# Performance work log

Measured on AMD Instinct MI355X. Metric: run time of the kernel, lower is better.

## Reference

```python
import jax, jax.numpy as jnp
import numpy as np

D_MODEL = 768
N_HEAD = 12


def setup_inputs() -> dict:
    key = jax.random.key(0)
    ks = jax.random.split(key, 5)
    B, S, D = 2, 4096, D_MODEL
    scale = 0.02
    return {
        "x": jax.random.normal(ks[0], (B, S, D), dtype=jnp.float32),
        "W_in": jax.random.normal(ks[1], (D, 3 * D), dtype=jnp.float32) * scale,
        "b_in": jax.random.normal(ks[2], (3 * D,), dtype=jnp.float32) * scale,
        "W_out": jax.random.normal(ks[3], (D, D), dtype=jnp.float32) * scale,
        "b_out": jax.random.normal(ks[4], (D,), dtype=jnp.float32) * scale,
    }


def reference(x, W_in, b_in, W_out, b_out):
    B, S, D = x.shape
    H = N_HEAD
    d_head = D // H
    qkv = x @ W_in + b_in                      # [B,S,3D]
    q, k, v = jnp.split(qkv, 3, axis=-1)
    # [B,H,S,d]
    q = q.reshape(B, S, H, d_head).transpose(0, 2, 1, 3)
    k = k.reshape(B, S, H, d_head).transpose(0, 2, 1, 3)
    v = v.reshape(B, S, H, d_head).transpose(0, 2, 1, 3)
    att = jnp.einsum("bhqd,bhkd->bhqk", q, k) * (1.0 / jnp.sqrt(jnp.float32(d_head)))
    causal = jnp.tril(jnp.ones((S, S), dtype=bool))
    att = jnp.where(causal[None, None], att, jnp.float32(-jnp.inf))
    att = jax.nn.softmax(att, axis=-1)
    y = jnp.einsum("bhqk,bhkd->bhqd", att, v)  # [B,H,S,d]
    y = y.transpose(0, 2, 1, 3).reshape(B, S, D)
    return y @ W_out + b_out
```

## Files before the change

### kernel.cpp

```cpp
#include <hip/hip_runtime.h>
#include <hip/hip_bf16.h>


#define D_MODEL 768
#define SEQ 4096
#define NB 2
#define NHEAD 12
#define LDQK 1536

typedef __attribute__((ext_vector_type(8))) short short8;
typedef __attribute__((ext_vector_type(4))) float floatx4;
typedef __attribute__((ext_vector_type(16))) float floatx16;

#define SM_C 0.18033688011112042f

#if __has_builtin(__builtin_amdgcn_exp2f)
#define EXP2(x) __builtin_amdgcn_exp2f(x)
#else
#define EXP2(x) __expf((x) * 0.6931471805599453f)
#endif

__device__ inline short fb(float f) {
    union { __hip_bfloat16 h; short s; } cv;
    cv.h = __float2bfloat16(f);
    return cv.s;
}
__device__ inline unsigned pk2(float a, float b) {
    float2 f; f.x = a; f.y = b;
    union { __hip_bfloat162 h; unsigned u; } cv;
    cv.h = __float22bfloat162_rn(f);
    return cv.u;
}
__device__ inline void gload16(const void* g, void* l) {
    __builtin_amdgcn_global_load_lds(
        (const __attribute__((address_space(1))) unsigned int*)g,
        (__attribute__((address_space(3))) unsigned int*)l, 16, 0, 0);
}

__global__ __launch_bounds__(256) void convert_bf16(const float* __restrict__ src,
                                                    short* __restrict__ dst, size_t n) {
    size_t i = ((size_t)blockIdx.x * 256 + threadIdx.x) * 8;
    if (i >= n) return;
    float4 f0 = *(const float4*)(src + i);
    float4 f1 = *(const float4*)(src + i + 4);
    uint4 u = {pk2(f0.x, f0.y), pk2(f0.z, f0.w), pk2(f1.x, f1.y), pk2(f1.z, f1.w)};
    *(uint4*)(dst + i) = u;
}

__global__ __launch_bounds__(256) void transpose_bf16(const float* __restrict__ W,
                                                      short* __restrict__ Wt,
                                                      int K, int N) {
    __shared__ short t[32][33];
    const int n0 = blockIdx.x * 32, k0 = blockIdx.y * 32;
    const int tx = threadIdx.x, ty = threadIdx.y;
#pragma unroll
    for (int j = 0; j < 4; ++j)
        t[ty + j * 8][tx] = fb(W[(size_t)(k0 + ty + j * 8) * N + n0 + tx]);
    __syncthreads();
#pragma unroll
    for (int j = 0; j < 4; ++j)
        Wt[(size_t)(n0 + ty + j * 8) * K + k0 + tx] = t[tx][ty + j * 8];
}

__global__ __launch_bounds__(256) void gemm_qkv128(const short* __restrict__ A,
                                                   const short* __restrict__ Bt,
                                                   const float* __restrict__ bias,
                                                   short* __restrict__ qkw,
                                                   short* __restrict__ vtw) {
    const int K = D_MODEL;
    __shared__ short As[128][32];
    __shared__ short Bs[128][32];
    const int tid = threadIdx.x, lane = tid & 63, w = tid >> 6;
    const int wr = w >> 1, wc = w & 1;
    const int lo = lane & 15, hi = lane >> 4;
    const int m0 = blockIdx.y * 128, n0 = blockIdx.x * 128;
    const int lr = lane >> 2, lc = (lane & 3) * 8;

    floatx4 acc[4][4] = {};
    const short* Ag = A  + (size_t)(m0 + w * 16 + lr) * K + lc;
    const short* Bg = Bt + (size_t)(n0 + w * 16 + lr) * K + lc;

    for (int k0 = 0; k0 < K; k0 += 32) {
        __syncthreads();
        gload16(Ag + k0,                  &As[w * 16][0]);
        gload16(Ag + k0 + (size_t)64 * K, &As[64 + w * 16][0]);
        gload16(Bg + k0,                  &Bs[w * 16][0]);
        gload16(Bg + k0 + (size_t)64 * K, &Bs[64 + w * 16][0]);
        __syncthreads();
        short8 a[4], bf[4];
#pragma unroll
        for (int m = 0; m < 4; ++m) a[m] = *(const short8*)&As[wr * 64 + m * 16 + lo][hi * 8];
#pragma unroll
        for (int n = 0; n < 4; ++n) bf[n] = *(const short8*)&Bs[wc * 64 + n * 16 + lo][hi * 8];
#pragma unroll
        for (int m = 0; m < 4; ++m)
#pragma unroll
            for (int n = 0; n < 4; ++n)
                acc[m][n] = __builtin_amdgcn_mfma_f32_16x16x32_bf16(a[m], bf[n], acc[m][n], 0, 0, 0);
    }

#pragma unroll
    for (int m = 0; m < 4; ++m)
#pragma unroll
        for (int n = 0; n < 4; ++n) {
            int col  = n0 + wc * 64 + n * 16 + lo;
            int row0 = m0 + wr * 64 + m * 16 + hi * 4;
            float bv = bias[col];
            if (col < LDQK) {
#pragma unroll
                for (int r = 0; r < 4; ++r) {
                    float v = acc[m][n][r] + bv;
                    if (col < D_MODEL) v *= SM_C;
                    qkw[(size_t)(row0 + r) * LDQK + col] = fb(v);
                }
            } else {
                int vcol = col - LDQK;
                int hh = vcol >> 6, dh = vcol & 63;
                int bb = row0 >> 12, s = row0 & 4095;
                uint2 u = {pk2(acc[m][n][0] + bv, acc[m][n][1] + bv),
                           pk2(acc[m][n][2] + bv, acc[m][n][3] + bv)};
                *(uint2*)&vtw[(((size_t)bb * NHEAD + hh) * 64 + dh) * SEQ + s] = u;
            }
        }
}

__global__ __launch_bounds__(256) void gemm_out128(const short* __restrict__ A,
                                                   const short* __restrict__ Bt,
                                                   const float* __restrict__ bias,
                                                   float* __restrict__ C) {
    const int K = D_MODEL, N = D_MODEL;
    __shared__ short As[128][32];
    __shared__ short Bs[128][32];
    const int tid = threadIdx.x, lane = tid & 63, w = tid >> 6;
    const int wr = w >> 1, wc = w & 1;
    const int lo = lane & 15, hi = lane >> 4;
    const int m0 = blockIdx.y * 128, n0 = blockIdx.x * 128;
    const int lr = lane >> 2, lc = (lane & 3) * 8;

    floatx4 acc[4][4] = {};
    const short* Ag = A  + (size_t)(m0 + w * 16 + lr) * K + lc;
    const short* Bg = Bt + (size_t)(n0 + w * 16 + lr) * K + lc;

    for (int k0 = 0; k0 < K; k0 += 32) {
        __syncthreads();
        gload16(Ag + k0,                  &As[w * 16][0]);
        gload16(Ag + k0 + (size_t)64 * K, &As[64 + w * 16][0]);
        gload16(Bg + k0,                  &Bs[w * 16][0]);
        gload16(Bg + k0 + (size_t)64 * K, &Bs[64 + w * 16][0]);
        __syncthreads();
        short8 a[4], bf[4];
#pragma unroll
        for (int m = 0; m < 4; ++m) a[m] = *(const short8*)&As[wr * 64 + m * 16 + lo][hi * 8];
#pragma unroll
        for (int n = 0; n < 4; ++n) bf[n] = *(const short8*)&Bs[wc * 64 + n * 16 + lo][hi * 8];
#pragma unroll
        for (int m = 0; m < 4; ++m)
#pragma unroll
            for (int n = 0; n < 4; ++n)
                acc[m][n] = __builtin_amdgcn_mfma_f32_16x16x32_bf16(a[m], bf[n], acc[m][n], 0, 0, 0);
    }

#pragma unroll
    for (int m = 0; m < 4; ++m)
#pragma unroll
        for (int n = 0; n < 4; ++n) {
            int col  = n0 + wc * 64 + n * 16 + lo;
            int row0 = m0 + wr * 64 + m * 16 + hi * 4;
            float bv = bias[col];
#pragma unroll
            for (int r = 0; r < 4; ++r)
                C[(size_t)(row0 + r) * N + col] = acc[m][n][r] + bv;
        }
}

__global__ __launch_bounds__(256, 3) void attn_k(const short* __restrict__ qk,
                                                 const short* __restrict__ vt,
                                                 short* __restrict__ y) {
    const int L = blockIdx.x;
    const int xcd = L & 7, slot = L >> 3;
    const int ghead = slot >> 5, ip = slot & 31;
    const int g = ghead * 8 + xcd;
    const int b = g / NHEAD, h = g % NHEAD;

    const int tid = threadIdx.x, lane = tid & 63, w = tid >> 6;
    const int q32 = lane & 31, hh = lane >> 5;
    const int pairB = w >> 1;
    const int wrow = (w & 1) * 32;

    __shared__ alignas(16) short KVs[2][2][64 * 64];
    __shared__ float Lcmb[128];

    const short* qbase = qk + (size_t)b * SEQ * LDQK;
    const short* kbase = qbase + D_MODEL;
    const short* vbase = vt + ((size_t)b * NHEAD + h) * 64 * SEQ;

    short* Kb = KVs[pairB][0];
    short* Vb = KVs[pairB][1];

    const int lt = tid & 127;
    const int srow = lt >> 1, shalf = lt & 1;
    int cof[4];
#pragma unroll
    for (int jj = 0; jj < 4; ++jj)
        cof[jj] = srow * 64 + ((shalf * 4 + jj) ^ (srow & 7)) * 8;

    const int qt_hi = 63 - ip, qt_lo = ip;
    int tq0 = (pairB ? qt_lo : qt_hi) * 64;

    short8 qf[4];
    {
        const short* qr = qbase + (size_t)(tq0 + wrow + q32) * LDQK + h * 64 + hh * 8;
        qf[0] = *(const short8*)(qr);
        qf[1] = *(const short8*)(qr + 16);
        qf[2] = *(const short8*)(qr + 32);
        qf[3] = *(const short8*)(qr + 48);
    }

    floatx16 O0 = {}, O1 = {};
    float lsum = 0.0f;

    short8 kpre[4], vpre[4];
    {
        const short* kg = kbase + (size_t)srow * LDQK + h * 64 + shalf * 32;
        const short* vg = vbase + (size_t)srow * SEQ + shalf * 32;
#pragma unroll
        for (int jj = 0; jj < 4; ++jj) {
            kpre[jj] = *(const short8*)(kg + jj * 8);
            vpre[jj] = *(const short8*)(vg + jj * 8);
        }
    }
    int curblk = 0;

    auto store_out = [&](float ltot) {
        float inv = 1.0f / ltot;
#pragma unroll
        for (int r = 0; r < 16; ++r) {
            int qrow = (r & 3) + 8 * (r >> 2) + 4 * hh;
            float iv = __shfl(inv, qrow, 64);
            short* d = y + ((size_t)b * SEQ + tq0 + wrow + qrow) * D_MODEL + h * 64;
            d[q32]      = fb(O0[r] * iv);
            d[32 + q32] = fb(O1[r] * iv);
        }
    };

    for (int j = 0; j <= 32; ++j) {
        __syncthreads();
        if (curblk >= 0) {
#pragma unroll
            for (int jj = 0; jj < 4; ++jj) {
                *(short8*)&Kb[cof[jj]] = kpre[jj];
                *(short8*)&Vb[cof[jj]] = vpre[jj];
            }
        }
        __syncthreads();

        int nxt;
        {
            int jn = j + 1;
            if (!pairB) nxt = (jn <= 32) ? jn : -1;
            else        nxt = (jn <= ip) ? jn : (jn <= 31 ? 32 + (jn - ip) : -1);
        }
        if (nxt >= 0) {
            const short* kg = kbase + (size_t)(nxt * 64 + srow) * LDQK + h * 64 + shalf * 32;
            const short* vg = vbase + (size_t)srow * SEQ + nxt * 64 + shalf * 32;
#pragma unroll
            for (int jj = 0; jj < 4; ++jj) {
                kpre[jj] = *(const short8*)(kg + jj * 8);
                vpre[jj] = *(const short8*)(vg + jj * 8);
            }
        }

        if (pairB && j == ip + 1) {
            float ltot = lsum + __shfl_xor(lsum, 32, 64);
            store_out(ltot);
#pragma unroll
            for (int r = 0; r < 16; ++r) { O0[r] = 0.0f; O1[r] = 0.0f; }
            lsum = 0.0f;
            tq0 = qt_hi * 64;
            const short* qr = qbase + (size_t)(tq0 + wrow + q32) * LDQK + h * 64 + hh * 8;
            qf[0] = *(const short8*)(qr);
            qf[1] = *(const short8*)(qr + 16);
            qf[2] = *(const short8*)(qr + 32);
            qf[3] = *(const short8*)(qr + 48);
        }

        if (curblk >= 0) {
            const int myqt = (pairB && j <= ip) ? qt_lo : qt_hi;
            const bool diag = (curblk == myqt);

#pragma unroll
            for (int kb2 = 0; kb2 < 2; ++kb2) {
                floatx16 S = {};
                __builtin_amdgcn_s_setprio(1);
#pragma unroll
                for (int kc = 0; kc < 4; ++kc) {
                    short8 kf = *(const short8*)&Kb[(kb2 * 32 + q32) * 64 + ((kc * 2 + hh) ^ (q32 & 7)) * 8];
                    S = __builtin_amdgcn_mfma_f32_32x32x16_bf16(kf, qf[kc], S, 0, 0, 0);
                }
                __builtin_amdgcn_s_setprio(0);

                if (diag) {
                    int qg = tq0 + wrow + q32;
                    int kb_base = curblk * 64 + kb2 * 32 + 4 * hh;
#pragma unroll
                    for (int r = 0; r < 16; ++r) {
                        int kgl = kb_base + (r & 3) + 8 * (r >> 2);
                        if (kgl > qg) S[r] = -1e30f;
                    }
                }

                unsigned wA[4], wB[4];
#pragma unroll
                for (int g4 = 0; g4 < 4; ++g4) {
                    float p0 = EXP2(S[4 * g4 + 0]), p1 = EXP2(S[4 * g4 + 1]);
                    float p2 = EXP2(S[4 * g4 + 2]), p3 = EXP2(S[4 * g4 + 3]);
                    lsum += (p0 + p1) + (p2 + p3);
                    wA[g4] = pk2(p0, p1);
                    wB[g4] = pk2(p2, p3);
                }
#pragma unroll
                for (int c16 = 0; c16 < 2; ++c16) {
                    unsigned xa = wA[2 * c16], ya = wA[2 * c16 + 1];
                    unsigned xb = wB[2 * c16], yb = wB[2 * c16 + 1];
                    asm("v_permlane32_swap_b32 %0, %1" : "+v"(xa), "+v"(ya));
                    asm("v_permlane32_swap_b32 %0, %1" : "+v"(xb), "+v"(yb));
                    union { unsigned u[4]; short8 s; } pa;
                    pa.u[0] = xa; pa.u[1] = xb; pa.u[2] = ya; pa.u[3] = yb;
                    const int kc = kb2 * 2 + c16;
                    short8 vf0 = *(const short8*)&Vb[q32 * 64 + ((kc * 2 + hh) ^ (q32 & 7)) * 8];
                    short8 vf1 = *(const short8*)&Vb[(32 + q32) * 64 + ((kc * 2 + hh) ^ (q32 & 7)) * 8];
                    __builtin_amdgcn_s_setprio(1);
                    O0 = __builtin_amdgcn_mfma_f32_32x32x16_bf16(pa.s, vf0, O0, 0, 0, 0);
                    O1 = __builtin_amdgcn_mfma_f32_32x32x16_bf16(pa.s, vf1, O1, 0, 0, 0);
                    __builtin_amdgcn_s_setprio(0);
                }
            }
        }
        curblk = nxt;
    }

    if (pairB) {
        float* cO = (float*)&KVs[1][0][0];
        const int lane2 = (w & 1) * 64 + lane;
#pragma unroll
        for (int r = 0; r < 16; ++r) {
            cO[r * 128 + lane2]        = O0[r];
            cO[(16 + r) * 128 + lane2] = O1[r];
        }
        Lcmb[lane2] = lsum;
    }
    __syncthreads();
    if (!pairB) {
        const float* cO = (const float*)&KVs[1][0][0];
        const int lane2 = (w & 1) * 64 + lane;
#pragma unroll
        for (int r = 0; r < 16; ++r) {
            O0[r] += cO[r * 128 + lane2];
            O1[r] += cO[(16 + r) * 128 + lane2];
        }
        lsum += Lcmb[lane2];
        float ltot = lsum + __shfl_xor(lsum, 32, 64);
        store_out(ltot);
    }
}

extern "C" void kernel_launch(void* const* d_in, const int* in_sizes, int n_in,
                              void* d_out, int out_size, void* d_ws, size_t ws_size,
                              hipStream_t stream) {
    (void)in_sizes; (void)n_in; (void)out_size; (void)ws_size;
    const float* x     = (const float*)d_in[0];
    const float* W_in  = (const float*)d_in[1];
    const float* b_in  = (const float*)d_in[2];
    const float* W_out = (const float*)d_in[3];
    const float* b_out = (const float*)d_in[4];
    float* out = (float*)d_out;

    const int M = NB * SEQ;
    char* p = (char*)d_ws;
    short* xbf   = (short*)p; p += (size_t)M * D_MODEL * 2;
    short* wtin  = (short*)p; p += (size_t)3 * D_MODEL * D_MODEL * 2;
    short* wtout = (short*)p; p += (size_t)D_MODEL * D_MODEL * 2;
    short* qkw   = (short*)p; p += (size_t)M * LDQK * 2;
    short* vtw   = (short*)p; p += (size_t)NB * NHEAD * 64 * SEQ * 2;
    short* yw    = (short*)p;

    convert_bf16<<<dim3((unsigned)((size_t)M * D_MODEL / 8 / 256)), 256, 0, stream>>>(
        x, xbf, (size_t)M * D_MODEL);
    transpose_bf16<<<dim3(3 * D_MODEL / 32, D_MODEL / 32), dim3(32, 8), 0, stream>>>(
        W_in, wtin, D_MODEL, 3 * D_MODEL);
    transpose_bf16<<<dim3(D_MODEL / 32, D_MODEL / 32), dim3(32, 8), 0, stream>>>(
        W_out, wtout, D_MODEL, D_MODEL);
    gemm_qkv128<<<dim3(3 * D_MODEL / 128, M / 128), 256, 0, stream>>>(
        xbf, wtin, b_in, qkw, vtw);
    attn_k<<<dim3(NB * NHEAD * (SEQ / 128)), 256, 0, stream>>>(qkw, vtw, yw);
    gemm_out128<<<dim3(D_MODEL / 128, M / 128), 256, 0, stream>>>(yw, wtout, b_out, out);
}
```

Baseline: 176.8 us.

## Pre-swizzle K/V into per-block tile images and stream them with direct LDS loads

The QKV GEMM epilogue now writes K and V into per-head, per-64-row block images that already carry the XOR swizzle used in shared memory, and Q into its own contiguous buffer. The attention kernel then copies each K/V block straight from global memory into LDS with gload16 instead of using register prefetch followed by swizzled LDS stores. This is meant to cut VGPR use and the register-to-LDS store instructions, and to make the global reads contiguous. In exchange, the register-staged prefetch of the next block, which overlapped the global load with compute, is gone, so load latency may be exposed between the two barriers. The K stores in the GEMM epilogue also become scattered 2-byte writes.

```diff
diff --git a/kernel.cpp b/kernel.cpp
--- a/kernel.cpp
+++ b/kernel.cpp
@@ -6,7 +6,6 @@
 #define SEQ 4096
 #define NB 2
 #define NHEAD 12
-#define LDQK 1536
 
 typedef __attribute__((ext_vector_type(8))) short short8;
 typedef __attribute__((ext_vector_type(4))) float floatx4;
@@ -65,8 +64,9 @@
 __global__ __launch_bounds__(256) void gemm_qkv128(const short* __restrict__ A,
                                                    const short* __restrict__ Bt,
                                                    const float* __restrict__ bias,
-                                                   short* __restrict__ qkw,
-                                                   short* __restrict__ vtw) {
+                                                   short* __restrict__ qw,
+                                                   short* __restrict__ kblk,
+                                                   short* __restrict__ vblk) {
     const int K = D_MODEL;
     __shared__ short As[128][32];
     __shared__ short Bs[128][32];
@@ -106,20 +106,31 @@
             int col  = n0 + wc * 64 + n * 16 + lo;
             int row0 = m0 + wr * 64 + m * 16 + hi * 4;
             float bv = bias[col];
-            if (col < LDQK) {
+            if (col < D_MODEL) {
+#pragma unroll
+                for (int r = 0; r < 4; ++r)
+                    qw[(size_t)(row0 + r) * D_MODEL + col] = fb((acc[m][n][r] + bv) * SM_C);
+            } else if (col < 2 * D_MODEL) {
+                int kc2 = col - D_MODEL;
+                int hh = kc2 >> 6, dh = kc2 & 63;
 #pragma unroll
                 for (int r = 0; r < 4; ++r) {
-                    float v = acc[m][n][r] + bv;
-                    if (col < D_MODEL) v *= SM_C;
-                    qkw[(size_t)(row0 + r) * LDQK + col] = fb(v);
+                    int row = row0 + r;
+                    int bb = row >> 12, s = row & 4095;
+                    int kb = s >> 6, kr = s & 63;
+                    size_t base = (((size_t)bb * NHEAD + hh) * 64 + kb) * 4096;
+                    kblk[base + kr * 64 + (((dh >> 3) ^ (kr & 7)) * 8) + (dh & 7)] =
+                        fb(acc[m][n][r] + bv);
                 }
             } else {
-                int vcol = col - LDQK;
+                int vcol = col - 2 * D_MODEL;
                 int hh = vcol >> 6, dh = vcol & 63;
                 int bb = row0 >> 12, s = row0 & 4095;
+                int kb = s >> 6, kr = s & 63;
+                size_t base = (((size_t)bb * NHEAD + hh) * 64 + kb) * 4096;
                 uint2 u = {pk2(acc[m][n][0] + bv, acc[m][n][1] + bv),
                            pk2(acc[m][n][2] + bv, acc[m][n][3] + bv)};
-                *(uint2*)&vtw[(((size_t)bb * NHEAD + hh) * 64 + dh) * SEQ + s] = u;
+                *(uint2*)&vblk[base + dh * 64 + (((kr >> 3) ^ (dh & 7)) * 8) + (kr & 7)] = u;
             }
         }
 }
@@ -173,8 +184,9 @@
         }
 }
 
-__global__ __launch_bounds__(256, 3) void attn_k(const short* __restrict__ qk,
-                                                 const short* __restrict__ vt,
+__global__ __launch_bounds__(256, 3) void attn_k(const short* __restrict__ qw,
+                                                 const short* __restrict__ kblk,
+                                                 const short* __restrict__ vblk,
                                                  short* __restrict__ y) {
     const int L = blockIdx.x;
     const int xcd = L & 7, slot = L >> 3;
@@ -185,31 +197,30 @@
     const int tid = threadIdx.x, lane = tid & 63, w = tid >> 6;
     const int q32 = lane & 31, hh = lane >> 5;
     const int pairB = w >> 1;
-    const int wrow = (w & 1) * 32;
+    const int wp = w & 1;
+    const int wrow = wp * 32;
 
     __shared__ alignas(16) short KVs[2][2][64 * 64];
     __shared__ float Lcmb[128];
 
-    const short* qbase = qk + (size_t)b * SEQ * LDQK;
-    const short* kbase = qbase + D_MODEL;
-    const short* vbase = vt + ((size_t)b * NHEAD + h) * 64 * SEQ;
+    const short* qbase = qw + (size_t)b * SEQ * D_MODEL;
+    const short* kimg = kblk + (((size_t)b * NHEAD + h) * 64) * 4096;
+    const short* vimg = vblk + (((size_t)b * NHEAD + h) * 64) * 4096;
 
     short* Kb = KVs[pairB][0];
     short* Vb = KVs[pairB][1];
 
-    const int lt = tid & 127;
-    const int srow = lt >> 1, shalf = lt & 1;
-    int cof[4];
-#pragma unroll
-    for (int jj = 0; jj < 4; ++jj)
-        cof[jj] = srow * 64 + ((shalf * 4 + jj) ^ (srow & 7)) * 8;
+    const short* kSrc = kimg + wp * 2048 + lane * 8;
+    const short* vSrc = vimg + wp * 2048 + lane * 8;
+    short* kDst = Kb + wp * 2048;
+    short* vDst = Vb + wp * 2048;
 
     const int qt_hi = 63 - ip, qt_lo = ip;
     int tq0 = (pairB ? qt_lo : qt_hi) * 64;
 
     short8 qf[4];
     {
-        const short* qr = qbase + (size_t)(tq0 + wrow + q32) * LDQK + h * 64 + hh * 8;
+        const short* qr = qbase + (size_t)(tq0 + wrow + q32) * D_MODEL + h * 64 + hh * 8;
         qf[0] = *(const short8*)(qr);
         qf[1] = *(const short8*)(qr + 16);
         qf[2] = *(const short8*)(qr + 32);
@@ -218,18 +229,6 @@
 
     floatx16 O0 = {}, O1 = {};
     float lsum = 0.0f;
-
-    short8 kpre[4], vpre[4];
-    {
-        const short* kg = kbase + (size_t)srow * LDQK + h * 64 + shalf * 32;
-        const short* vg = vbase + (size_t)srow * SEQ + shalf * 32;
-#pragma unroll
-        for (int jj = 0; jj < 4; ++jj) {
-            kpre[jj] = *(const short8*)(kg + jj * 8);
-            vpre[jj] = *(const short8*)(vg + jj * 8);
-        }
-    }
-    int curblk = 0;
 
     auto store_out = [&](float ltot) {
         float inv = 1.0f / ltot;
@@ -244,31 +243,21 @@
     };
 
     for (int j = 0; j <= 32; ++j) {
-        __syncthreads();
-        if (curblk >= 0) {
-#pragma unroll
-            for (int jj = 0; jj < 4; ++jj) {
-                *(short8*)&Kb[cof[jj]] = kpre[jj];
-                *(short8*)&Vb[cof[jj]] = vpre[jj];
+        int myblk;
+        if (!pairB) myblk = j;
+        else        myblk = (j <= ip) ? j : (j <= 31 ? 32 + (j - ip) : -1);
+
+        __syncthreads();
+        if (myblk >= 0) {
+            const short* ks = kSrc + (size_t)myblk * 4096;
+            const short* vs = vSrc + (size_t)myblk * 4096;
+#pragma unroll
+            for (int c = 0; c < 4; ++c) {
+                gload16(ks + c * 512, kDst + c * 512);
+                gload16(vs + c * 512, vDst + c * 512);
             }
         }
         __syncthreads();
-
-        int nxt;
-        {
-            int jn = j + 1;
-            if (!pairB) nxt = (jn <= 32) ? jn : -1;
-            else        nxt = (jn <= ip) ? jn : (jn <= 31 ? 32 + (jn - ip) : -1);
-        }
-        if (nxt >= 0) {
-            const short* kg = kbase + (size_t)(nxt * 64 + srow) * LDQK + h * 64 + shalf * 32;
-            const short* vg = vbase + (size_t)srow * SEQ + nxt * 64 + shalf * 32;
-#pragma unroll
-            for (int jj = 0; jj < 4; ++jj) {
-                kpre[jj] = *(const short8*)(kg + jj * 8);
-                vpre[jj] = *(const short8*)(vg + jj * 8);
-            }
-        }
 
         if (pairB && j == ip + 1) {
             float ltot = lsum + __shfl_xor(lsum, 32, 64);
@@ -277,16 +266,16 @@
             for (int r = 0; r < 16; ++r) { O0[r] = 0.0f; O1[r] = 0.0f; }
             lsum = 0.0f;
             tq0 = qt_hi * 64;
-            const short* qr = qbase + (size_t)(tq0 + wrow + q32) * LDQK + h * 64 + hh * 8;
+            const short* qr = qbase + (size_t)(tq0 + wrow + q32) * D_MODEL + h * 64 + hh * 8;
             qf[0] = *(const short8*)(qr);
             qf[1] = *(const short8*)(qr + 16);
             qf[2] = *(const short8*)(qr + 32);
             qf[3] = *(const short8*)(qr + 48);
         }
 
-        if (curblk >= 0) {
+        if (myblk >= 0) {
             const int myqt = (pairB && j <= ip) ? qt_lo : qt_hi;
-            const bool diag = (curblk == myqt);
+            const bool diag = (myblk == myqt);
 
 #pragma unroll
             for (int kb2 = 0; kb2 < 2; ++kb2) {
@@ -301,7 +290,7 @@
 
                 if (diag) {
                     int qg = tq0 + wrow + q32;
-                    int kb_base = curblk * 64 + kb2 * 32 + 4 * hh;
+                    int kb_base = myblk * 64 + kb2 * 32 + 4 * hh;
 #pragma unroll
                     for (int r = 0; r < 16; ++r) {
                         int kgl = kb_base + (r & 3) + 8 * (r >> 2);
@@ -336,12 +325,11 @@
                 }
             }
         }
-        curblk = nxt;
     }
 
     if (pairB) {
         float* cO = (float*)&KVs[1][0][0];
-        const int lane2 = (w & 1) * 64 + lane;
+        const int lane2 = wp * 64 + lane;
 #pragma unroll
         for (int r = 0; r < 16; ++r) {
             cO[r * 128 + lane2]        = O0[r];
@@ -352,7 +340,7 @@
     __syncthreads();
     if (!pairB) {
         const float* cO = (const float*)&KVs[1][0][0];
-        const int lane2 = (w & 1) * 64 + lane;
+        const int lane2 = wp * 64 + lane;
 #pragma unroll
         for (int r = 0; r < 16; ++r) {
             O0[r] += cO[r * 128 + lane2];
@@ -380,8 +368,9 @@
     short* xbf   = (short*)p; p += (size_t)M * D_MODEL * 2;
     short* wtin  = (short*)p; p += (size_t)3 * D_MODEL * D_MODEL * 2;
     short* wtout = (short*)p; p += (size_t)D_MODEL * D_MODEL * 2;
-    short* qkw   = (short*)p; p += (size_t)M * LDQK * 2;
-    short* vtw   = (short*)p; p += (size_t)NB * NHEAD * 64 * SEQ * 2;
+    short* qw    = (short*)p; p += (size_t)M * D_MODEL * 2;
+    short* kblk  = (short*)p; p += (size_t)NB * NHEAD * 64 * 4096 * 2;
+    short* vblk  = (short*)p; p += (size_t)NB * NHEAD * 64 * 4096 * 2;
     short* yw    = (short*)p;
 
     convert_bf16<<<dim3((unsigned)((size_t)M * D_MODEL / 8 / 256)), 256, 0, stream>>>(
@@ -391,7 +380,7 @@
     transpose_bf16<<<dim3(D_MODEL / 32, D_MODEL / 32), dim3(32, 8), 0, stream>>>(
         W_out, wtout, D_MODEL, D_MODEL);
     gemm_qkv128<<<dim3(3 * D_MODEL / 128, M / 128), 256, 0, stream>>>(
-        xbf, wtin, b_in, qkw, vtw);
-    attn_k<<<dim3(NB * NHEAD * (SEQ / 128)), 256, 0, stream>>>(qkw, vtw, yw);
+        xbf, wtin, b_in, qw, kblk, vblk);
+    attn_k<<<dim3(NB * NHEAD * (SEQ / 128)), 256, 0, stream>>>(qw, kblk, vblk, yw);
     gemm_out128<<<dim3(D_MODEL / 128, M / 128), 256, 0, stream>>>(yw, wtout, b_out, out);
 }
```

Measured after the change: 171.2 us. 1.03x faster.
